# Kernel optimization log

Measured on AMD Instinct MI355X. Metric: run time of the kernel, lower is better.

The kernel has to match this reference:

```python
import jax, jax.numpy as jnp
import numpy as np


def conv2d(x, w, b, pad=0, groups=1):
    y = jax.lax.conv_general_dilated(
        x, w, (1, 1), [(pad, pad), (pad, pad)],
        dimension_numbers=('NCHW', 'OIHW', 'NCHW'), feature_group_count=groups)
    return y + b[None, :, None, None]


def layernorm(x, w, b, eps=1e-5):
    # per-pixel LayerNorm over channel dim (matches to_3d -> nn.LayerNorm(dim) -> to_4d)
    mu = x.mean(1, keepdims=True)
    var = ((x - mu) ** 2).mean(1, keepdims=True)
    return (x - mu) * jax.lax.rsqrt(var + eps) * w[None, :, None, None] + b[None, :, None, None]


def setup_inputs():
    key = jax.random.key(0)
    ks = jax.random.split(key, 16)
    B, C, H, W = 1, 64, 64, 64
    heads, dh = 8, 8
    inner = heads * dh          # 64
    hid_lc = 32                 # max(16, inner // 2)
    hid_f = 4 * C               # 256, ffn_expansion_factor = 4
    def s(k, shape, fan):
        return (jax.random.normal(k, shape, jnp.float32) / np.float32(np.sqrt(fan)))
    return {
        'x': jax.random.normal(ks[0], (B, C, H, W), jnp.float32),
        'luma': jax.random.uniform(ks[1], (B, 1, H, W), jnp.float32),
        'ln1_w': jnp.ones((C,), jnp.float32), 'ln1_b': jnp.zeros((C,), jnp.float32),
        'qkv_w': s(ks[2], (3 * inner, C, 1, 1), C), 'qkv_b': jnp.zeros((3 * inner,), jnp.float32),
        'proj_w': s(ks[3], (C, inner, 1, 1), inner), 'proj_b': jnp.zeros((C,), jnp.float32),
        'lc1_w': s(ks[4], (hid_lc, 1, 3, 3), 9), 'lc1_b': jnp.zeros((hid_lc,), jnp.float32),
        'lc2_w': s(ks[5], (hid_lc, hid_lc, 3, 3), 9 * hid_lc), 'lc2_b': jnp.zeros((hid_lc,), jnp.float32),
        'gam_w': s(ks[6], (inner, hid_lc, 1, 1), hid_lc), 'gam_b': jnp.zeros((inner,), jnp.float32),
        'bet_w': s(ks[7], (inner, hid_lc, 1, 1), hid_lc), 'bet_b': jnp.zeros((inner,), jnp.float32),
        'alpha': jnp.float32(0.1),
        'ln2_w': jnp.ones((C,), jnp.float32), 'ln2_b': jnp.zeros((C,), jnp.float32),
        'ffn1_w': s(ks[8], (hid_f, C, 1, 1), C), 'ffn1_b': jnp.zeros((hid_f,), jnp.float32),
        'dw_w': s(ks[9], (hid_f, 1, 3, 3), 9), 'dw_b': jnp.zeros((hid_f,), jnp.float32),
        'ffn2_w': s(ks[10], (C, hid_f, 1, 1), hid_f), 'ffn2_b': jnp.zeros((C,), jnp.float32),
    }


def reference(x, luma, ln1_w, ln1_b, qkv_w, qkv_b, proj_w, proj_b,
              lc1_w, lc1_b, lc2_w, lc2_b, gam_w, gam_b, bet_w, bet_b, alpha,
              ln2_w, ln2_b, ffn1_w, ffn1_b, dw_w, dw_b, ffn2_w, ffn2_b):
    B, C, H, W = x.shape
    heads = 8
    N = H * W
    # --- attention branch ---
    xn = layernorm(x, ln1_w, ln1_b)
    qkv = conv2d(xn, qkv_w, qkv_b)             # [B, 3*inner, H, W]
    inner = qkv.shape[1] // 3
    dh = inner // heads

    def to_bhnd(t):  # b (h d) x y -> b h (x y) d
        return t.reshape(B, heads, dh, N).transpose(0, 1, 3, 2)

    q, k, v = [to_bhnd(t) for t in jnp.split(qkv, 3, axis=1)]
    # luma conditioning
    h1 = jax.nn.relu(conv2d(luma, lc1_w, lc1_b, pad=1))
    h1 = jax.nn.relu(conv2d(h1, lc2_w, lc2_b, pad=1))
    g = to_bhnd(conv2d(h1, gam_w, gam_b))
    bt = to_bhnd(conv2d(h1, bet_w, bet_b))
    q = g * q + bt
    k = g * k + bt
    v = g * v + bt
    # additive luma bias on q (avg_pool2d 3x3, count_include_pad=True -> fixed /9)
    invL = 1.0 - luma
    invL = jax.lax.reduce_window(invL, 0.0, jax.lax.add, (1, 1, 3, 3), (1, 1, 1, 1),
                                 [(0, 0), (0, 0), (1, 1), (1, 1)]) / 9.0
    invL = invL.reshape(B, N)
    invL = invL - invL.mean(-1, keepdims=True)
    q = q + alpha * invL[:, None, :, None]
    scale = dh ** -0.5
    attn = jax.nn.softmax(jnp.einsum('bhid,bhjd->bhij', q, k) * scale, axis=-1)
    out = jnp.einsum('bhij,bhjd->bhid', attn, v)
    out = out.transpose(0, 1, 3, 2).reshape(B, inner, H, W)
    x = x + conv2d(out, proj_w, proj_b)
    # --- ConvFFN branch ---
    y = layernorm(x, ln2_w, ln2_b)
    y = conv2d(y, ffn1_w, ffn1_b)
    y = conv2d(y, dw_w, dw_b, pad=1, groups=y.shape[1])
    y = jax.nn.gelu(y, approximate=False)
    y = conv2d(y, ffn2_w, ffn2_b)
    return x + y
```

## Files before the change

### kernel.cpp

```cpp
#include <hip/hip_runtime.h>
#include <math.h>

#define NPIX 4096
#define IMG 64

typedef __attribute__((ext_vector_type(8))) short bf16x8;
typedef __attribute__((ext_vector_type(4))) float floatx4;
typedef __attribute__((ext_vector_type(4))) unsigned int uintx4;

__device__ __forceinline__ unsigned int split_pack(float x) {
  unsigned int u = __float_as_uint(x);
  unsigned int hif = u & 0xffff0000u;
  float lof = x - __uint_as_float(hif);
  return (u >> 16) | (__float_as_uint(lof) & 0xffff0000u);
}

__device__ __forceinline__ unsigned int pack_hi2(float a, float b) {
  return __builtin_amdgcn_perm(__float_as_uint(b), __float_as_uint(a),
                               0x07060302u);
}

__global__ __launch_bounds__(256) void lc12_kernel(
    const float* __restrict__ luma, const float* __restrict__ w1,
    const float* __restrict__ b1, const float* __restrict__ w2,
    const float* __restrict__ b2, const float* __restrict__ x,
    float* __restrict__ h2, float* __restrict__ pooled,
    float* __restrict__ bsums, float* __restrict__ mu1,
    float* __restrict__ rs1, unsigned short* __restrict__ cbuf) {
  __shared__ float lum[400];
  __shared__ float sw1[288];
  __shared__ float tin[32][324];
  __shared__ float swt[4][32][9];
  __shared__ float red[256];
  int tile = blockIdx.x, ocg = blockIdx.y;
  int ty0 = (tile >> 2) * 16, tx0 = (tile & 3) * 16;
  int tid = threadIdx.x;
  if (tile == 0 && ocg == 0 && tid < 16) cbuf[tid] = (tid < 8) ? 0x3F80 : 0;
  for (int idx = tid; idx < 400; idx += 256) {
    int py = idx / 20, px = idx - py * 20;
    int gy = ty0 + py - 2, gx = tx0 + px - 2;
    lum[idx] = (gy >= 0 && gy < IMG && gx >= 0 && gx < IMG)
                   ? luma[gy * IMG + gx]
                   : 0.f;
  }
  for (int idx = tid; idx < 288; idx += 256) sw1[idx] = w1[idx];
  for (int idx = tid; idx < 1152; idx += 256) {
    int o = idx / 288, r = idx - o * 288;
    swt[o][r / 9][r % 9] = w2[(ocg * 4 + o) * 288 + r];
  }
  __syncthreads();
  for (int idx = tid; idx < 32 * 324; idx += 256) {
    int ic = idx / 324, pos = idx - ic * 324;
    int py = pos / 18, px = pos - py * 18;
    int gy = ty0 + py - 1, gx = tx0 + px - 1;
    float v = 0.f;
    if (gy >= 0 && gy < IMG && gx >= 0 && gx < IMG) {
      float s = b1[ic];
      const float* wp = &sw1[ic * 9];
#pragma unroll
      for (int dy = 0; dy < 3; dy++)
#pragma unroll
        for (int dx = 0; dx < 3; dx++)
          s = fmaf(wp[dy * 3 + dx], lum[(py + dy) * 20 + px + dx], s);
      v = fmaxf(s, 0.f);
    }
    tin[ic][pos] = v;
  }
  __syncthreads();
  int ly = tid >> 4, lx = tid & 15;
  int p = (ty0 + ly) * IMG + tx0 + lx;
  float acc[4];
#pragma unroll
  for (int o = 0; o < 4; o++) acc[o] = b2[ocg * 4 + o];
  for (int ic = 0; ic < 32; ic++) {
    float v[9];
#pragma unroll
    for (int dy = 0; dy < 3; dy++)
#pragma unroll
      for (int dx = 0; dx < 3; dx++)
        v[dy * 3 + dx] = tin[ic][(ly + dy) * 18 + lx + dx];
#pragma unroll
    for (int o = 0; o < 4; o++)
#pragma unroll
      for (int t = 0; t < 9; t++) acc[o] = fmaf(swt[o][ic][t], v[t], acc[o]);
  }
#pragma unroll
  for (int o = 0; o < 4; o++)
    h2[(ocg * 4 + o) * NPIX + p] = fmaxf(acc[o], 0.f);
  if (ocg == 0) {
    int gy = ty0 + ly, gx = tx0 + lx;
    float sv = 0.f;
#pragma unroll
    for (int dy = 0; dy < 3; dy++)
#pragma unroll
      for (int dx = 0; dx < 3; dx++)
        sv += lum[(ly + dy + 1) * 20 + lx + dx + 1];
    float cy = 3.f - (gy == 0 ? 1.f : 0.f) - (gy == 63 ? 1.f : 0.f);
    float cx = 3.f - (gx == 0 ? 1.f : 0.f) - (gx == 63 ? 1.f : 0.f);
    float pv = (cy * cx - sv) * (1.f / 9.f);
    pooled[p] = pv;
    red[tid] = pv;
    __syncthreads();
    for (int st = 128; st > 0; st >>= 1) {
      if (tid < st) red[tid] += red[tid + st];
      __syncthreads();
    }
    if (tid == 0) bsums[tile] = red[0];
    float s = 0.f, q = 0.f;
#pragma unroll 8
    for (int cc = 0; cc < 64; cc++) {
      float xv = x[cc * NPIX + p];
      s += xv;
      q = fmaf(xv, xv, q);
    }
    float mu = s * (1.f / 64.f);
    mu1[p] = mu;
    rs1[p] = rsqrtf(q * (1.f / 64.f) - mu * mu + 1e-5f);
  }
}

__global__ __launch_bounds__(256) void ln_qkv_kernel(
    const float* __restrict__ X, const float* __restrict__ mu1,
    const float* __restrict__ rs1, const float* __restrict__ lnw,
    const float* __restrict__ lnb, const float* __restrict__ W,
    const float* __restrict__ bias, const float* __restrict__ gamW,
    const float* __restrict__ gamB, const float* __restrict__ betW,
    const float* __restrict__ betB, const float* __restrict__ h2,
    const float* __restrict__ pooled, const float* __restrict__ bsums,
    const float* __restrict__ alpha, unsigned short* __restrict__ qhl,
    unsigned short* __restrict__ khl, unsigned short* __restrict__ vthx,
    unsigned short* __restrict__ vtlx) {
  const float QSCALE = 0.35355339059327376f * 1.4426950408889634f;
  __shared__ float xs[64][32];
  __shared__ float wsh[64][64];
  __shared__ float h2s[32][32];
  __shared__ float wgs[32][64];
  __shared__ float wbs[32][64];
  __shared__ float mu[32];
  __shared__ float rs[32];
  int n0 = blockIdx.x * 32, part = blockIdx.y, m0 = part * 64;
  int tid = threadIdx.x;
  if (tid < 32) {
    mu[tid] = mu1[n0 + tid];
    rs[tid] = rs1[n0 + tid];
  }
  {
    int e = tid * 2;
    int c = e >> 3, off = (e & 7) * 4;
    *(float4*)&xs[c][off] = *(const float4*)&X[c * NPIX + n0 + off];
    int e1 = e + 1;
    int c1 = e1 >> 3, off1 = (e1 & 7) * 4;
    *(float4*)&xs[c1][off1] = *(const float4*)&X[c1 * NPIX + n0 + off1];
  }
  {
    int m = tid >> 2, kg = (tid & 3) * 16;
    const float4* wr = (const float4*)&W[(m0 + m) * 64 + kg];
    float4 w0 = wr[0], w1 = wr[1], w2 = wr[2], w3 = wr[3];
    float wv[16] = {w0.x, w0.y, w0.z, w0.w, w1.x, w1.y, w1.z, w1.w,
                    w2.x, w2.y, w2.z, w2.w, w3.x, w3.y, w3.z, w3.w};
#pragma unroll
    for (int j = 0; j < 16; j++) wsh[kg + j][m] = wv[j];
  }
  {
    int k = tid >> 3, nf = (tid & 7) * 4;
    *(float4*)&h2s[k][nf] = *(const float4*)&h2[k * NPIX + n0 + nf];
  }
  {
    int m = tid >> 2, kg = (tid & 3) * 8;
    const float4* g0 = (const float4*)&gamW[m * 32 + kg];
    float4 a = g0[0], b4 = g0[1];
    float gv[8] = {a.x, a.y, a.z, a.w, b4.x, b4.y, b4.z, b4.w};
#pragma unroll
    for (int j = 0; j < 8; j++) wgs[kg + j][m] = gv[j];
    const float4* bb0 = (const float4*)&betW[m * 32 + kg];
    float4 c4 = bb0[0], d4 = bb0[1];
    float bv[8] = {c4.x, c4.y, c4.z, c4.w, d4.x, d4.y, d4.z, d4.w};
#pragma unroll
    for (int j = 0; j < 8; j++) wbs[kg + j][m] = bv[j];
  }
  __syncthreads();
  {
    int c = tid >> 2, pg = (tid & 3) * 8;
    float wc = lnw[c], bc = lnb[c];
#pragma unroll
    for (int j = 0; j < 8; j++) {
      int p = pg + j;
      xs[c][p] = (xs[c][p] - mu[p]) * rs[p] * wc + bc;
    }
  }
  __syncthreads();
  int tx = tid & 15, ty = tid >> 4;
  float ga[4][2] = {}, ba[4][2] = {};
#pragma unroll 8
  for (int kk = 0; kk < 32; kk++) {
    float4 wg4 = *(const float4*)&wgs[kk][ty * 4];
    float4 wb4 = *(const float4*)&wbs[kk][ty * 4];
    float2 h22 = *(const float2*)&h2s[kk][tx * 2];
    float gv[4] = {wg4.x, wg4.y, wg4.z, wg4.w};
    float bv[4] = {wb4.x, wb4.y, wb4.z, wb4.w};
    float hv[2] = {h22.x, h22.y};
#pragma unroll
    for (int im = 0; im < 4; im++)
#pragma unroll
      for (int in = 0; in < 2; in++) {
        ga[im][in] = fmaf(gv[im], hv[in], ga[im][in]);
        ba[im][in] = fmaf(bv[im], hv[in], ba[im][in]);
      }
  }
#pragma unroll
  for (int im = 0; im < 4; im++) {
    int cc = ty * 4 + im;
    float gb = gamB[cc], bb2 = betB[cc];
#pragma unroll
    for (int in = 0; in < 2; in++) {
      ga[im][in] += gb;
      ba[im][in] += bb2;
    }
  }
  float acc[4][2] = {};
#pragma unroll 8
  for (int kk = 0; kk < 64; kk++) {
    float4 a = *(const float4*)&wsh[kk][ty * 4];
    float2 b2 = *(const float2*)&xs[kk][tx * 2];
    float av[4] = {a.x, a.y, a.z, a.w};
    float bv[2] = {b2.x, b2.y};
#pragma unroll
    for (int im = 0; im < 4; im++)
#pragma unroll
      for (int in = 0; in < 2; in++)
        acc[im][in] = fmaf(av[im], bv[in], acc[im][in]);
  }
  float val[4][2];
#pragma unroll
  for (int im = 0; im < 4; im++) {
    int cc = ty * 4 + im;
    float bv = bias[m0 + cc];
#pragma unroll
    for (int in = 0; in < 2; in++)
      val[im][in] = fmaf(ga[im][in], acc[im][in] + bv, ba[im][in]);
  }
  if (part == 0) {
    float msum = 0.f;
#pragma unroll
    for (int t = 0; t < 16; t++) msum += bsums[t];
    float mean = msum * (1.f / 4096.f);
    float a0 = alpha[0];
    const float2 pv = *(const float2*)&pooled[n0 + tx * 2];
    float iv[2] = {a0 * (pv.x - mean), a0 * (pv.y - mean)};
#pragma unroll
    for (int im = 0; im < 4; im++)
#pragma unroll
      for (int in = 0; in < 2; in++)
        val[im][in] = (val[im][in] + iv[in]) * QSCALE;
  }
  if (part < 2) {
    unsigned short* dst = (part == 0) ? qhl : khl;
    int h = ty >> 1, d0 = (ty & 1) * 4;
#pragma unroll
    for (int in = 0; in < 2; in++) {
      int n = n0 + tx * 2 + in;
      unsigned int pk[4];
#pragma unroll
      for (int im = 0; im < 4; im++) pk[im] = split_pack(val[im][in]);
      short4 hi, lo;
      hi.x = (short)(pk[0] & 0xffffu); hi.y = (short)(pk[1] & 0xffffu);
      hi.z = (short)(pk[2] & 0xffffu); hi.w = (short)(pk[3] & 0xffffu);
      lo.x = (short)(pk[0] >> 16); lo.y = (short)(pk[1] >> 16);
      lo.z = (short)(pk[2] >> 16); lo.w = (short)(pk[3] >> 16);
      unsigned short* base = dst + ((size_t)(h * NPIX + n) << 4) + d0;
      *(short4*)base = hi;
      *(short4*)(base + 8) = lo;
    }
  } else {
    int nq = n0 + tx * 2;
    int off0 = (nq >> 5) * 32 + ((nq >> 4) & 1) * 4 + ((nq >> 2) & 3) * 8 +
               (nq & 3);
#pragma unroll
    for (int im = 0; im < 4; im++) {
      int cc = ty * 4 + im;
      unsigned int pk0 = split_pack(val[im][0]);
      unsigned int pk1 = split_pack(val[im][1]);
      short2 hi, lo;
      hi.x = (short)(pk0 & 0xffffu);
      hi.y = (short)(pk1 & 0xffffu);
      lo.x = (short)(pk0 >> 16);
      lo.y = (short)(pk1 >> 16);
      *(short2*)(vthx + (size_t)cc * NPIX + off0) = hi;
      *(short2*)(vtlx + (size_t)cc * NPIX + off0) = lo;
    }
  }
}

__global__ __launch_bounds__(256, 4) void attn_kernel(
    const unsigned short* __restrict__ qhl,
    const unsigned short* __restrict__ khl,
    const unsigned short* __restrict__ vthx,
    const unsigned short* __restrict__ vtlx,
    const unsigned short* __restrict__ cbuf, float* __restrict__ pacc,
    float* __restrict__ pl) {
  int tid = threadIdx.x;
  int wave = tid >> 6, lane = tid & 63;
  int g = lane >> 4, c = lane & 15;
  int h = blockIdx.y, jp = blockIdx.z;
  int i0 = blockIdx.x * 256 + wave * 64;
  int jbase = jp * 512;
  bf16x8 qB[4];
#pragma unroll
  for (int t = 0; t < 4; t++)
    qB[t] = *(const bf16x8*)(qhl + ((size_t)(h * NPIX + i0 + t * 16 + c) << 4) +
                             ((g & 1) << 3));
  const unsigned short* kp =
      khl + ((size_t)(h * NPIX + jbase + c) << 4) + ((g >> 1) << 3);
  const unsigned short* vhp;
  const unsigned short* vlp;
  int vstep;
  if (c < 8) {
    vhp = vthx + (size_t)(h * 8 + c) * NPIX + jbase + (g << 3);
    vlp = vtlx + (size_t)(h * 8 + c) * NPIX + jbase + (g << 3);
    vstep = 32;
  } else {
    vhp = (c == 8) ? cbuf : (cbuf + 8);
    vlp = cbuf + 8;
    vstep = 0;
  }
  floatx4 zero4 = {0.f, 0.f, 0.f, 0.f};
  floatx4 aH[4], aM[4];
#pragma unroll
  for (int t = 0; t < 4; t++) {
    aH[t] = zero4;
    aM[t] = zero4;
  }
#pragma unroll 4
  for (int jt = 0; jt < 16; ++jt) {
    bf16x8 ka0 = *(const bf16x8*)kp;
    bf16x8 ka1 = *(const bf16x8*)(kp + 256);
    bf16x8 avh = *(const bf16x8*)vhp;
    bf16x8 avl = *(const bf16x8*)vlp;
    kp += 512;
    vhp += vstep;
    vlp += vstep;
#pragma unroll
    for (int t = 0; t < 4; t++) {
      floatx4 s0 =
          __builtin_amdgcn_mfma_f32_16x16x32_bf16(ka0, qB[t], zero4, 0, 0, 0);
      floatx4 s1 =
          __builtin_amdgcn_mfma_f32_16x16x32_bf16(ka1, qB[t], zero4, 0, 0, 0);
      float p0 = __builtin_amdgcn_exp2f(fminf(s0[0], 80.f));
      float p1 = __builtin_amdgcn_exp2f(fminf(s0[1], 80.f));
      float p2 = __builtin_amdgcn_exp2f(fminf(s0[2], 80.f));
      float p3 = __builtin_amdgcn_exp2f(fminf(s0[3], 80.f));
      float p4 = __builtin_amdgcn_exp2f(fminf(s1[0], 80.f));
      float p5 = __builtin_amdgcn_exp2f(fminf(s1[1], 80.f));
      float p6 = __builtin_amdgcn_exp2f(fminf(s1[2], 80.f));
      float p7 = __builtin_amdgcn_exp2f(fminf(s1[3], 80.f));
      uintx4 bh;
      bh.x = pack_hi2(p0, p1);
      bh.y = pack_hi2(p2, p3);
      bh.z = pack_hi2(p4, p5);
      bh.w = pack_hi2(p6, p7);
      bf16x8 pbh = __builtin_bit_cast(bf16x8, bh);
      aH[t] = __builtin_amdgcn_mfma_f32_16x16x32_bf16(avh, pbh, aH[t], 0, 0, 0);
      aM[t] = __builtin_amdgcn_mfma_f32_16x16x32_bf16(avl, pbh, aM[t], 0, 0, 0);
    }
  }
#pragma unroll
  for (int t = 0; t < 4; t++) {
    floatx4 o = aH[t] + aM[t];
    if (g < 2) {
      size_t b0 = (size_t)((jp * 8 + h) * NPIX + i0 + t * 16 + c);
      *(float4*)&pacc[b0 * 8 + g * 4] = make_float4(o[0], o[1], o[2], o[3]);
    } else if (g == 2) {
      pl[(size_t)((jp * 8 + h) * NPIX + i0 + t * 16 + c)] = o[0];
    }
  }
}

__global__ __launch_bounds__(256) void proj_ffn1_kernel(
    const float* __restrict__ pacc, const float* __restrict__ pl,
    const float* __restrict__ Wp, const float* __restrict__ bp,
    const float* __restrict__ x, const float* __restrict__ ln2w,
    const float* __restrict__ ln2b, const float* __restrict__ W1,
    const float* __restrict__ b1f, float* __restrict__ x1,
    float* __restrict__ f1) {
  __shared__ float at[64][34];
  __shared__ float wsh[64][68];
  __shared__ float w1s[64][68];
  __shared__ float xsl[64][34];
  __shared__ float ps[16][34];
  __shared__ float pq[16][34];
  __shared__ float mus[32];
  __shared__ float rss[32];
  int n0 = blockIdx.x * 32;
  int ch = blockIdx.y;
  int tid = threadIdx.x;
  {
    int mm = tid >> 2, kg = (tid & 3) * 16;
    const float4* wr = (const float4*)&Wp[mm * 64 + kg];
    float4 w0 = wr[0], w1 = wr[1], w2 = wr[2], w3 = wr[3];
    float wv[16] = {w0.x, w0.y, w0.z, w0.w, w1.x, w1.y, w1.z, w1.w,
                    w2.x, w2.y, w2.z, w2.w, w3.x, w3.y, w3.z, w3.w};
#pragma unroll
    for (int j = 0; j < 16; j++) wsh[kg + j][mm] = wv[j];
    const float4* w1r = (const float4*)&W1[(ch * 64 + mm) * 64 + kg];
    float4 u0 = w1r[0], u1 = w1r[1], u2 = w1r[2], u3 = w1r[3];
    float uv[16] = {u0.x, u0.y, u0.z, u0.w, u1.x, u1.y, u1.z, u1.w,
                    u2.x, u2.y, u2.z, u2.w, u3.x, u3.y, u3.z, u3.w};
#pragma unroll
    for (int j = 0; j < 16; j++) w1s[kg + j][mm] = uv[j];
  }
  {
    int hh = tid >> 5, nn = tid & 31;
    int i = n0 + nn;
    float L = 0.f, o[8] = {};
#pragma unroll
    for (int p = 0; p < 8; p++) {
      size_t base = (size_t)((p * 8 + hh) * NPIX + i);
      L += pl[base];
      const float4 a0 = *(const float4*)&pacc[base * 8];
      const float4 a1 = *(const float4*)&pacc[base * 8 + 4];
      o[0] += a0.x; o[1] += a0.y; o[2] += a0.z; o[3] += a0.w;
      o[4] += a1.x; o[5] += a1.y; o[6] += a1.z; o[7] += a1.w;
    }
    float inv = 1.f / L;
#pragma unroll
    for (int d = 0; d < 8; d++) at[hh * 8 + d][nn] = o[d] * inv;
  }
  __syncthreads();
  int mq = tid >> 4, pp = (tid & 15) * 2;
  float acc[4][2] = {};
#pragma unroll 8
  for (int k = 0; k < 64; k++) {
    float4 w4 = *(const float4*)&wsh[k][mq * 4];
    float2 b2 = *(const float2*)&at[k][pp];
    acc[0][0] = fmaf(w4.x, b2.x, acc[0][0]);
    acc[0][1] = fmaf(w4.x, b2.y, acc[0][1]);
    acc[1][0] = fmaf(w4.y, b2.x, acc[1][0]);
    acc[1][1] = fmaf(w4.y, b2.y, acc[1][1]);
    acc[2][0] = fmaf(w4.z, b2.x, acc[2][0]);
    acc[2][1] = fmaf(w4.z, b2.y, acc[2][1]);
    acc[3][0] = fmaf(w4.w, b2.x, acc[3][0]);
    acc[3][1] = fmaf(w4.w, b2.y, acc[3][1]);
  }
  float v[4][2], sn0 = 0.f, sn1 = 0.f, qn0 = 0.f, qn1 = 0.f;
#pragma unroll
  for (int im = 0; im < 4; im++) {
    int row = mq * 4 + im;
    float bpv = bp[row];
    const float2 xr = *(const float2*)&x[row * NPIX + n0 + pp];
    float v0 = acc[im][0] + bpv + xr.x;
    float v1 = acc[im][1] + bpv + xr.y;
    v[im][0] = v0;
    v[im][1] = v1;
    sn0 += v0;
    qn0 = fmaf(v0, v0, qn0);
    sn1 += v1;
    qn1 = fmaf(v1, v1, qn1);
  }
  if (ch == 0) {
#pragma unroll
    for (int im = 0; im < 4; im++)
      *(float2*)&x1[(mq * 4 + im) * NPIX + n0 + pp] =
          make_float2(v[im][0], v[im][1]);
  }
  ps[mq][pp] = sn0;
  ps[mq][pp + 1] = sn1;
  pq[mq][pp] = qn0;
  pq[mq][pp + 1] = qn1;
  __syncthreads();
  if (tid < 32) {
    float s = 0.f, q = 0.f;
#pragma unroll
    for (int t = 0; t < 16; t++) {
      s += ps[t][tid];
      q += pq[t][tid];
    }
    float mu = s * (1.f / 64.f);
    mus[tid] = mu;
    rss[tid] = rsqrtf(q * (1.f / 64.f) - mu * mu + 1e-5f);
  }
  __syncthreads();
  {
    float mu0 = mus[pp], mu1v = mus[pp + 1];
    float rs0 = rss[pp], rs1v = rss[pp + 1];
#pragma unroll
    for (int im = 0; im < 4; im++) {
      int row = mq * 4 + im;
      float w2v = ln2w[row], b2v = ln2b[row];
      *(float2*)&xsl[row][pp] =
          make_float2((v[im][0] - mu0) * rs0 * w2v + b2v,
                      (v[im][1] - mu1v) * rs1v * w2v + b2v);
    }
  }
  __syncthreads();
  float a2[4][2] = {};
#pragma unroll 8
  for (int k = 0; k < 64; k++) {
    float4 w4 = *(const float4*)&w1s[k][mq * 4];
    float2 b2 = *(const float2*)&xsl[k][pp];
    a2[0][0] = fmaf(w4.x, b2.x, a2[0][0]);
    a2[0][1] = fmaf(w4.x, b2.y, a2[0][1]);
    a2[1][0] = fmaf(w4.y, b2.x, a2[1][0]);
    a2[1][1] = fmaf(w4.y, b2.y, a2[1][1]);
    a2[2][0] = fmaf(w4.z, b2.x, a2[2][0]);
    a2[2][1] = fmaf(w4.z, b2.y, a2[2][1]);
    a2[3][0] = fmaf(w4.w, b2.x, a2[3][0]);
    a2[3][1] = fmaf(w4.w, b2.y, a2[3][1]);
  }
#pragma unroll
  for (int im = 0; im < 4; im++) {
    int row = ch * 64 + mq * 4 + im;
    float bb = b1f[row];
    *(float2*)&f1[row * NPIX + n0 + pp] =
        make_float2(a2[im][0] + bb, a2[im][1] + bb);
  }
}

__global__ __launch_bounds__(256) void ffn2_dw_kernel(
    const float* __restrict__ f1, const float* __restrict__ dww,
    const float* __restrict__ dwb, const float* __restrict__ W,
    const float* __restrict__ bias, const float* __restrict__ resid,
    float* __restrict__ C) {
  __shared__ float xs2[16][260];
  __shared__ float wshT[32][260];
  int n0 = blockIdx.x * 16, m0 = blockIdx.y * 32;
  int tid = threadIdx.x;
  int y = n0 >> 6, x0 = n0 & 63;
  {
    int mm = tid >> 3, kg = (tid & 7) * 32;
    const float4* src = (const float4*)&W[(m0 + mm) * 256 + kg];
    float4* dst = (float4*)&wshT[mm][kg];
#pragma unroll
    for (int i = 0; i < 8; i++) dst[i] = src[i];
  }
  {
    int px4 = (tid & 3) * 4;
    int xabs = x0 + px4;
#pragma unroll
    for (int k = 0; k < 4; k++) {
      int c = (tid >> 2) + 64 * k;
      const float* base = f1 + c * NPIX;
      float wv[9];
#pragma unroll
      for (int i = 0; i < 9; i++) wv[i] = dww[c * 9 + i];
      float bc = dwb[c];
      float a[4] = {bc, bc, bc, bc};
#pragma unroll
      for (int dy = 0; dy < 3; dy++) {
        int yy = y + dy - 1;
        if (yy < 0 || yy > 63) continue;
        const float* row = base + yy * IMG + xabs;
        float4 mid = *(const float4*)row;
        float left = (xabs > 0) ? row[-1] : 0.f;
        float right = (xabs + 4 < IMG) ? row[4] : 0.f;
        float win[6] = {left, mid.x, mid.y, mid.z, mid.w, right};
#pragma unroll
        for (int o = 0; o < 4; o++)
#pragma unroll
          for (int dx = 0; dx < 3; dx++)
            a[o] = fmaf(wv[dy * 3 + dx], win[o + dx], a[o]);
      }
#pragma unroll
      for (int o = 0; o < 4; o++)
        xs2[px4 + o][c] =
            0.5f * a[o] * (1.f + erff(a[o] * 0.70710678118654752f));
    }
  }
  __syncthreads();
  int m = tid >> 3, np = (tid & 7) * 2;
  float a0 = 0.f, a1 = 0.f;
#pragma unroll 4
  for (int k4 = 0; k4 < 64; k4++) {
    float4 w4 = *(const float4*)&wshT[m][k4 * 4];
    float4 xa = *(const float4*)&xs2[np][k4 * 4];
    float4 xb = *(const float4*)&xs2[np + 1][k4 * 4];
    a0 = fmaf(w4.x, xa.x, a0);
    a1 = fmaf(w4.x, xb.x, a1);
    a0 = fmaf(w4.y, xa.y, a0);
    a1 = fmaf(w4.y, xb.y, a1);
    a0 = fmaf(w4.z, xa.z, a0);
    a1 = fmaf(w4.z, xb.z, a1);
    a0 = fmaf(w4.w, xa.w, a0);
    a1 = fmaf(w4.w, xb.w, a1);
  }
  int row = m0 + m;
  float bv = bias[row];
  const float2 rr = *(const float2*)&resid[row * NPIX + n0 + np];
  *(float2*)&C[row * NPIX + n0 + np] =
      make_float2(a0 + bv + rr.x, a1 + bv + rr.y);
}

extern "C" void kernel_launch(void* const* d_in, const int* in_sizes, int n_in,
                              void* d_out, int out_size, void* d_ws,
                              size_t ws_size, hipStream_t stream) {
  const float* x      = (const float*)d_in[0];
  const float* luma   = (const float*)d_in[1];
  const float* ln1_w  = (const float*)d_in[2];
  const float* ln1_b  = (const float*)d_in[3];
  const float* qkv_w  = (const float*)d_in[4];
  const float* qkv_b  = (const float*)d_in[5];
  const float* proj_w = (const float*)d_in[6];
  const float* proj_b = (const float*)d_in[7];
  const float* lc1_w  = (const float*)d_in[8];
  const float* lc1_b  = (const float*)d_in[9];
  const float* lc2_w  = (const float*)d_in[10];
  const float* lc2_b  = (const float*)d_in[11];
  const float* gam_w  = (const float*)d_in[12];
  const float* gam_b  = (const float*)d_in[13];
  const float* bet_w  = (const float*)d_in[14];
  const float* bet_b  = (const float*)d_in[15];
  const float* alpha  = (const float*)d_in[16];
  const float* ln2_w  = (const float*)d_in[17];
  const float* ln2_b  = (const float*)d_in[18];
  const float* ffn1_w = (const float*)d_in[19];
  const float* ffn1_b = (const float*)d_in[20];
  const float* dw_w   = (const float*)d_in[21];
  const float* dw_b   = (const float*)d_in[22];
  const float* ffn2_w = (const float*)d_in[23];
  const float* ffn2_b = (const float*)d_in[24];
  float* out = (float*)d_out;

  float* w = (float*)d_ws;
  float* pooled = w + 0;
  float* bsums  = w + 4096;
  unsigned short* cbuf = (unsigned short*)(w + 4160);
  float* mu1 = w + 4224;
  float* rs1 = w + 8320;
  unsigned short* qhl  = (unsigned short*)(w + 12416);
  unsigned short* khl  = (unsigned short*)(w + 274560);
  unsigned short* vthx = (unsigned short*)(w + 536704);
  unsigned short* vtlx = (unsigned short*)(w + 667776);
  float* pacc = w + 798848;
  float* pl   = w + 2896000;
  float* x1   = w + 3158144;
  float* f1   = w + 3420288;
  float* h2   = w + 4468864;

  lc12_kernel<<<dim3(16, 8), 256, 0, stream>>>(luma, lc1_w, lc1_b, lc2_w,
                                               lc2_b, x, h2, pooled, bsums,
                                               mu1, rs1, cbuf);
  ln_qkv_kernel<<<dim3(128, 3), 256, 0, stream>>>(
      x, mu1, rs1, ln1_w, ln1_b, qkv_w, qkv_b, gam_w, gam_b, bet_w, bet_b, h2,
      pooled, bsums, alpha, qhl, khl, vthx, vtlx);
  attn_kernel<<<dim3(16, 8, 8), 256, 0, stream>>>(qhl, khl, vthx, vtlx, cbuf,
                                                  pacc, pl);
  proj_ffn1_kernel<<<dim3(128, 4), 256, 0, stream>>>(
      pacc, pl, proj_w, proj_b, x, ln2_w, ln2_b, ffn1_w, ffn1_b, x1, f1);
  ffn2_dw_kernel<<<dim3(256, 2), 256, 0, stream>>>(f1, dw_w, dw_b, ffn2_w,
                                                   ffn2_b, x1, out);
}
```

Before: 190.7 us.

## Compute LN1 stats inside qkv kernel and halve attention key splits

The LayerNorm-1 per-pixel mean and rstd are now computed inside ln_qkv_kernel from the x tile already staged in shared memory, so lc12_kernel no longer re-reads x and no mu1/rs1 buffers are written or read. Separately, the attention key dimension is split into 4 chunks of 1024 instead of 8 of 512. That halves the partial accumulators written and reduced in proj_ffn1, at the cost of fewer blocks (512 instead of 1024) and a longer serial loop per block.

New measurement: 192.4 us. About the same (+0.9%).

```diff
diff --git a/kernel.cpp b/kernel.cpp
--- a/kernel.cpp
+++ b/kernel.cpp
@@ -23,10 +23,9 @@
 __global__ __launch_bounds__(256) void lc12_kernel(
     const float* __restrict__ luma, const float* __restrict__ w1,
     const float* __restrict__ b1, const float* __restrict__ w2,
-    const float* __restrict__ b2, const float* __restrict__ x,
-    float* __restrict__ h2, float* __restrict__ pooled,
-    float* __restrict__ bsums, float* __restrict__ mu1,
-    float* __restrict__ rs1, unsigned short* __restrict__ cbuf) {
+    const float* __restrict__ b2, float* __restrict__ h2,
+    float* __restrict__ pooled, float* __restrict__ bsums,
+    unsigned short* __restrict__ cbuf) {
   __shared__ float lum[400];
   __shared__ float sw1[288];
   __shared__ float tin[32][324];
@@ -106,22 +105,11 @@
       __syncthreads();
     }
     if (tid == 0) bsums[tile] = red[0];
-    float s = 0.f, q = 0.f;
-#pragma unroll 8
-    for (int cc = 0; cc < 64; cc++) {
-      float xv = x[cc * NPIX + p];
-      s += xv;
-      q = fmaf(xv, xv, q);
-    }
-    float mu = s * (1.f / 64.f);
-    mu1[p] = mu;
-    rs1[p] = rsqrtf(q * (1.f / 64.f) - mu * mu + 1e-5f);
   }
 }
 
 __global__ __launch_bounds__(256) void ln_qkv_kernel(
-    const float* __restrict__ X, const float* __restrict__ mu1,
-    const float* __restrict__ rs1, const float* __restrict__ lnw,
+    const float* __restrict__ X, const float* __restrict__ lnw,
     const float* __restrict__ lnb, const float* __restrict__ W,
     const float* __restrict__ bias, const float* __restrict__ gamW,
     const float* __restrict__ gamB, const float* __restrict__ betW,
@@ -136,14 +124,12 @@
   __shared__ float h2s[32][32];
   __shared__ float wgs[32][64];
   __shared__ float wbs[32][64];
+  __shared__ float pss[8][32];
+  __shared__ float pqq[8][32];
   __shared__ float mu[32];
   __shared__ float rs[32];
   int n0 = blockIdx.x * 32, part = blockIdx.y, m0 = part * 64;
   int tid = threadIdx.x;
-  if (tid < 32) {
-    mu[tid] = mu1[n0 + tid];
-    rs[tid] = rs1[n0 + tid];
-  }
   {
     int e = tid * 2;
     int c = e >> 3, off = (e & 7) * 4;
@@ -177,6 +163,31 @@
     float bv[8] = {c4.x, c4.y, c4.z, c4.w, d4.x, d4.y, d4.z, d4.w};
 #pragma unroll
     for (int j = 0; j < 8; j++) wbs[kg + j][m] = bv[j];
+  }
+  __syncthreads();
+  {
+    int p = tid & 31, i = tid >> 5;
+    float s = 0.f, q = 0.f;
+#pragma unroll
+    for (int j = 0; j < 8; j++) {
+      float xv = xs[i * 8 + j][p];
+      s += xv;
+      q = fmaf(xv, xv, q);
+    }
+    pss[i][p] = s;
+    pqq[i][p] = q;
+  }
+  __syncthreads();
+  if (tid < 32) {
+    float s = 0.f, q = 0.f;
+#pragma unroll
+    for (int i = 0; i < 8; i++) {
+      s += pss[i][tid];
+      q += pqq[i][tid];
+    }
+    float m = s * (1.f / 64.f);
+    mu[tid] = m;
+    rs[tid] = rsqrtf(q * (1.f / 64.f) - m * m + 1e-5f);
   }
   __syncthreads();
   {
@@ -303,7 +314,7 @@
   int g = lane >> 4, c = lane & 15;
   int h = blockIdx.y, jp = blockIdx.z;
   int i0 = blockIdx.x * 256 + wave * 64;
-  int jbase = jp * 512;
+  int jbase = jp * 1024;
   bf16x8 qB[4];
 #pragma unroll
   for (int t = 0; t < 4; t++)
@@ -331,7 +342,7 @@
     aM[t] = zero4;
   }
 #pragma unroll 4
-  for (int jt = 0; jt < 16; ++jt) {
+  for (int jt = 0; jt < 32; ++jt) {
     bf16x8 ka0 = *(const bf16x8*)kp;
     bf16x8 ka1 = *(const bf16x8*)(kp + 256);
     bf16x8 avh = *(const bf16x8*)vhp;
@@ -413,7 +424,7 @@
     int i = n0 + nn;
     float L = 0.f, o[8] = {};
 #pragma unroll
-    for (int p = 0; p < 8; p++) {
+    for (int p = 0; p < 4; p++) {
       size_t base = (size_t)((p * 8 + hh) * NPIX + i);
       L += pl[base];
       const float4 a0 = *(const float4*)&pacc[base * 8];
@@ -623,8 +634,6 @@
   float* pooled = w + 0;
   float* bsums  = w + 4096;
   unsigned short* cbuf = (unsigned short*)(w + 4160);
-  float* mu1 = w + 4224;
-  float* rs1 = w + 8320;
   unsigned short* qhl  = (unsigned short*)(w + 12416);
   unsigned short* khl  = (unsigned short*)(w + 274560);
   unsigned short* vthx = (unsigned short*)(w + 536704);
@@ -636,12 +645,11 @@
   float* h2   = w + 4468864;
 
   lc12_kernel<<<dim3(16, 8), 256, 0, stream>>>(luma, lc1_w, lc1_b, lc2_w,
-                                               lc2_b, x, h2, pooled, bsums,
-                                               mu1, rs1, cbuf);
+                                               lc2_b, h2, pooled, bsums, cbuf);
   ln_qkv_kernel<<<dim3(128, 3), 256, 0, stream>>>(
-      x, mu1, rs1, ln1_w, ln1_b, qkv_w, qkv_b, gam_w, gam_b, bet_w, bet_b, h2,
+      x, ln1_w, ln1_b, qkv_w, qkv_b, gam_w, gam_b, bet_w, bet_b, h2,
       pooled, bsums, alpha, qhl, khl, vthx, vtlx);
-  attn_kernel<<<dim3(16, 8, 8), 256, 0, stream>>>(qhl, khl, vthx, vtlx, cbuf,
+  attn_kernel<<<dim3(16, 8, 4), 256, 0, stream>>>(qhl, khl, vthx, vtlx, cbuf,
                                                   pacc, pl);
   proj_ffn1_kernel<<<dim3(128, 4), 256, 0, stream>>>(
       pacc, pl, proj_w, proj_b, x, ln2_w, ln2_b, ffn1_w, ffn1_b, x1, f1);
```
